# Kernel tuning notes

Measured on AMD Instinct MI355X. Metric: run time of the kernel, lower is better.

The kernel has to match this reference:

```python
import jax, jax.numpy as jnp
import numpy as np

N_NODES = 50000


def setup_inputs() -> dict:
    key = jax.random.key(0)
    k1, k2, k3, k4 = jax.random.split(key, 4)
    in_f, out_f = 128, 128
    n_edges = 625000
    x = jax.random.normal(k1, (N_NODES, in_f), dtype=jnp.float32)
    index = jax.random.randint(k2, (2, n_edges), 0, N_NODES, dtype=jnp.int64)
    # reset_parameters uses uniform(-1/sqrt(in), 1/sqrt(in))
    bound = 1.0 / np.sqrt(in_f)
    weight = jax.random.uniform(k3, (in_f, out_f), minval=-bound, maxval=bound, dtype=jnp.float32)
    bias = jax.random.uniform(k4, (out_f,), minval=-bound, maxval=bound, dtype=jnp.float32)
    return {"x": x, "index": index, "weight": weight, "bias": bias}


def reference(x, index, weight, bias):
    # F_out = D_hat^{-1/2} (A + I) D_hat^{-1/2} X W + b
    n = x.shape[0]
    loops = jnp.arange(n, dtype=index.dtype)
    src = jnp.concatenate([index[0], loops])  # [E + N]
    dst = jnp.concatenate([index[1], loops])
    # degrees of A_hat (counted on destination nodes)
    deg = jax.ops.segment_sum(jnp.ones_like(dst, dtype=x.dtype), dst, num_segments=n)
    dinv = jax.lax.rsqrt(jnp.maximum(deg, 1e-12))
    norm = dinv[src] * dinv[dst]  # [E + N]
    h = x @ weight  # [N, out] dense GEMM first (out <= in)
    msg = h[src] * norm[:, None]  # gather + scale
    out = jax.ops.segment_sum(msg, dst, num_segments=n)  # scatter-add
    return out + bias
```

## Files before the change

### kernel.cpp

```cpp
#include <hip/hip_runtime.h>

#define F   128
#define PAD 64

typedef short short8 __attribute__((ext_vector_type(8)));
typedef float f32x4v __attribute__((ext_vector_type(4)));

__device__ __forceinline__ ushort f2bf(float f) {
    uint b = __float_as_uint(f);
    uint r = (b + 0x7fffu + ((b >> 16) & 1u)) >> 16;
    return (ushort)r;
}
__device__ __forceinline__ float bflo(uint v) { return __uint_as_float(v << 16); }
__device__ __forceinline__ float bfhi(uint v) { return __uint_as_float(v & 0xffff0000u); }


__global__ __launch_bounds__(256) void prep(
    const float* __restrict__ w, ushort* __restrict__ wt,
    int* __restrict__ cnt, int n)
{
    int i = blockIdx.x * 256 + threadIdx.x;
    if (i < n) cnt[i] = 0;
    if (blockIdx.x == 0) {
        for (int idx = threadIdx.x; idx < F * 32; idx += 256) {
            int k = idx >> 5, c4 = idx & 31;
            float4 v = *reinterpret_cast<const float4*>(&w[k * F + c4 * 4]);
            wt[(c4 * 4 + 0) * F + k] = f2bf(v.x);
            wt[(c4 * 4 + 1) * F + k] = f2bf(v.y);
            wt[(c4 * 4 + 2) * F + k] = f2bf(v.z);
            wt[(c4 * 4 + 3) * F + k] = f2bf(v.w);
        }
    }
}


__global__ __launch_bounds__(256) void hybrid(
    const int* __restrict__ src, const int* __restrict__ dst, int ne,
    int* __restrict__ cnt, int* __restrict__ padded, int nbB,
    const float* __restrict__ x, const ushort* __restrict__ wt,
    ushort* __restrict__ g, int n)
{
    __shared__ ushort sX[64 * F];
    __shared__ ushort sW[F * F];

    if (blockIdx.x < nbB) {
        int base = (blockIdx.x * 256 + threadIdx.x) * 4;
        if (base + 3 < ne) {
            int4 s4 = *reinterpret_cast<const int4*>(&src[base]);
            int4 d4 = *reinterpret_cast<const int4*>(&dst[base]);
            int p;
            p = atomicAdd(&cnt[d4.x], 1); if (p < PAD) padded[(size_t)d4.x * PAD + p] = s4.x;
            p = atomicAdd(&cnt[d4.y], 1); if (p < PAD) padded[(size_t)d4.y * PAD + p] = s4.y;
            p = atomicAdd(&cnt[d4.z], 1); if (p < PAD) padded[(size_t)d4.z * PAD + p] = s4.z;
            p = atomicAdd(&cnt[d4.w], 1); if (p < PAD) padded[(size_t)d4.w * PAD + p] = s4.w;
        } else {
            for (int e = base; e < ne; ++e) {
                int s = src[e], d = dst[e];
                int p = atomicAdd(&cnt[d], 1);
                if (p < PAD) padded[(size_t)d * PAD + p] = s;
            }
        }
        return;
    }

    const int t    = threadIdx.x;
    const int lane = t & 63;
    const int wv   = t >> 6;
    const int row0 = (blockIdx.x - nbB) * 64;

    for (int i = t; i < 2048; i += 256) {
        int col = i >> 4, k8 = i & 15;
        short8 v = *reinterpret_cast<const short8*>(&wt[col * F + k8 * 8]);
        int byte = col * 256 + k8 * 16;
        byte ^= (col & 7) << 4;
        *reinterpret_cast<short8*>((char*)sW + byte) = v;
    }
    for (int i = t; i < 2048; i += 256) {
        int r = i >> 5, c4 = i & 31;
        int row = row0 + r;
        float4 v = make_float4(0.f, 0.f, 0.f, 0.f);
        if (row < n) v = *reinterpret_cast<const float4*>(&x[(size_t)row * F + c4 * 4]);
        ushort u[4] = {f2bf(v.x), f2bf(v.y), f2bf(v.z), f2bf(v.w)};
        int byte = r * 256 + c4 * 8;
        byte ^= (r & 7) << 4;
        *reinterpret_cast<uint2*>((char*)sX + byte) = *reinterpret_cast<uint2*>(u);
    }
    __syncthreads();

    const int l15 = lane & 15, kg = lane >> 4;

    short8 af[4][4];
    #pragma unroll
    for (int rt = 0; rt < 4; ++rt)
        #pragma unroll
        for (int kt = 0; kt < 4; ++kt) {
            int row = rt * 16 + l15;
            int byte = row * 256 + kt * 64 + kg * 16;
            byte ^= (row & 7) << 4;
            af[rt][kt] = *reinterpret_cast<const short8*>((const char*)sX + byte);
        }

    const int wc = wv * 32;
    short8 bfr[2][4];
    #pragma unroll
    for (int ct = 0; ct < 2; ++ct)
        #pragma unroll
        for (int kt = 0; kt < 4; ++kt) {
            int col = wc + ct * 16 + l15;
            int byte = col * 256 + kt * 64 + kg * 16;
            byte ^= (col & 7) << 4;
            bfr[ct][kt] = *reinterpret_cast<const short8*>((const char*)sW + byte);
        }

    f32x4v acc[4][2];
    #pragma unroll
    for (int rt = 0; rt < 4; ++rt)
        #pragma unroll
        for (int ct = 0; ct < 2; ++ct)
            acc[rt][ct] = (f32x4v){0.f, 0.f, 0.f, 0.f};

    #pragma unroll
    for (int kt = 0; kt < 4; ++kt)
        #pragma unroll
        for (int rt = 0; rt < 4; ++rt)
            #pragma unroll
            for (int ct = 0; ct < 2; ++ct)
                acc[rt][ct] = __builtin_amdgcn_mfma_f32_16x16x32_bf16(
                    af[rt][kt], bfr[ct][kt], acc[rt][ct], 0, 0, 0);

    #pragma unroll
    for (int rt = 0; rt < 4; ++rt) {
        int rbase = row0 + rt * 16 + kg * 4;
        #pragma unroll
        for (int ct = 0; ct < 2; ++ct) {
            int col = wc + ct * 16 + l15;
            #pragma unroll
            for (int rr = 0; rr < 4; ++rr) {
                int row = rbase + rr;
                if (row < n)
                    g[(size_t)row * F + col] = f2bf(acc[rt][ct][rr]);
            }
        }
    }
}


__global__ __launch_bounds__(256) void gather_bf16(
    const int* __restrict__ cnt, const int* __restrict__ padded,
    const ushort* __restrict__ g, const float* __restrict__ bias,
    float* __restrict__ out, int n)
{
    int wid  = (blockIdx.x * 256 + threadIdx.x) >> 6;
    int lane = threadIdx.x & 63;
    if (wid >= n) return;
    const int c = lane * 2;

    int   cv = cnt[wid];
    float dv = rsqrtf((float)cv + 1.0f);
    uint self = *reinterpret_cast<const uint*>(&g[(size_t)wid * F + c]);
    float ax = dv * bflo(self), ay = dv * bfhi(self);

    int m = cv < PAD ? cv : PAD;
    const int* pl = padded + (size_t)wid * PAD;

    int j = 0;
    for (; j + 4 <= m; j += 4) {
        int s0 = pl[j + 0], s1 = pl[j + 1], s2 = pl[j + 2], s3 = pl[j + 3];
        float d0 = rsqrtf((float)cnt[s0] + 1.0f);
        float d1 = rsqrtf((float)cnt[s1] + 1.0f);
        float d2 = rsqrtf((float)cnt[s2] + 1.0f);
        float d3 = rsqrtf((float)cnt[s3] + 1.0f);
        uint v0 = *reinterpret_cast<const uint*>(&g[(size_t)s0 * F + c]);
        uint v1 = *reinterpret_cast<const uint*>(&g[(size_t)s1 * F + c]);
        uint v2 = *reinterpret_cast<const uint*>(&g[(size_t)s2 * F + c]);
        uint v3 = *reinterpret_cast<const uint*>(&g[(size_t)s3 * F + c]);
        ax = fmaf(d0, bflo(v0), ax); ay = fmaf(d0, bfhi(v0), ay);
        ax = fmaf(d1, bflo(v1), ax); ay = fmaf(d1, bfhi(v1), ay);
        ax = fmaf(d2, bflo(v2), ax); ay = fmaf(d2, bfhi(v2), ay);
        ax = fmaf(d3, bflo(v3), ax); ay = fmaf(d3, bfhi(v3), ay);
    }
    for (; j < m; ++j) {
        int s = pl[j];
        float ds = rsqrtf((float)cnt[s] + 1.0f);
        uint v = *reinterpret_cast<const uint*>(&g[(size_t)s * F + c]);
        ax = fmaf(ds, bflo(v), ax);
        ay = fmaf(ds, bfhi(v), ay);
    }

    float2 bb = *reinterpret_cast<const float2*>(&bias[c]);
    float2 o;
    o.x = fmaf(dv, ax, bb.x);
    o.y = fmaf(dv, ay, bb.y);
    *reinterpret_cast<float2*>(&out[(size_t)wid * F + c]) = o;
}


__global__ __launch_bounds__(256) void gemm_scale(
    const float* __restrict__ x, const float* __restrict__ w,
    const float* __restrict__ dinv, float* __restrict__ g, int n)
{
    __shared__ float sWl[F * F];
    __shared__ float sXl[8][F];
    for (int i = threadIdx.x; i < F * F; i += 256) sWl[i] = w[i];
    __syncthreads();
    const int r  = threadIdx.x >> 5;
    const int cg = threadIdx.x & 31;
    for (int row0 = blockIdx.x * 8; row0 < n; row0 += gridDim.x * 8) {
        {
            int t4 = threadIdx.x * 4;
            int rr = t4 >> 7, cc = t4 & (F - 1);
            if (row0 + rr < n) {
                float4 v = *reinterpret_cast<const float4*>(&x[(size_t)(row0 + rr) * F + cc]);
                *reinterpret_cast<float4*>(&sXl[rr][cc]) = v;
            }
        }
        __syncthreads();
        int row = row0 + r;
        if (row < n) {
            float4 acc = make_float4(0.f, 0.f, 0.f, 0.f);
            const float* xr = sXl[r];
            #pragma unroll 8
            for (int k = 0; k < F; ++k) {
                float  xv = xr[k];
                float4 wv = *reinterpret_cast<const float4*>(&sWl[k * F + cg * 4]);
                acc.x = fmaf(xv, wv.x, acc.x);
                acc.y = fmaf(xv, wv.y, acc.y);
                acc.z = fmaf(xv, wv.z, acc.z);
                acc.w = fmaf(xv, wv.w, acc.w);
            }
            float s = dinv[row];
            acc.x *= s; acc.y *= s; acc.z *= s; acc.w *= s;
            *reinterpret_cast<float4*>(&g[(size_t)row * F + cg * 4]) = acc;
        }
        __syncthreads();
    }
}

__global__ void init_degf(float* __restrict__ deg, int n) {
    int i = blockIdx.x * blockDim.x + threadIdx.x;
    if (i < n) deg[i] = 1.0f;
}
__global__ void count_degf(const int* __restrict__ dst, int ne, float* __restrict__ deg) {
    int e = blockIdx.x * blockDim.x + threadIdx.x;
    if (e < ne) atomicAdd(&deg[dst[e]], 1.0f);
}
__global__ void calc_dinvf(const float* __restrict__ deg, float* __restrict__ dinv, int n) {
    int i = blockIdx.x * blockDim.x + threadIdx.x;
    if (i < n) dinv[i] = rsqrtf(fmaxf(deg[i], 1e-12f));
}
__global__ __launch_bounds__(256) void scatter_edges(
    const int* __restrict__ src, const int* __restrict__ dst, int ne,
    const float* __restrict__ g, float* __restrict__ out)
{
    int gid  = (blockIdx.x * blockDim.x + threadIdx.x) >> 5;
    int lane = threadIdx.x & 31;
    if (gid >= ne) return;
    int s = src[gid], d = dst[gid];
    float4 v = *reinterpret_cast<const float4*>(&g[(size_t)s * F + lane * 4]);
    float* op = &out[(size_t)d * F + lane * 4];
    atomicAdd(op + 0, v.x);
    atomicAdd(op + 1, v.y);
    atomicAdd(op + 2, v.z);
    atomicAdd(op + 3, v.w);
}
__global__ __launch_bounds__(256) void finalize(
    float* __restrict__ out, const float* __restrict__ g,
    const float* __restrict__ dinv, const float* __restrict__ bias, int n)
{
    int i = blockIdx.x * blockDim.x + threadIdx.x;
    if (i >= n * 32) return;
    int row = i >> 5, c4 = i & 31;
    float  s = dinv[row];
    float4 o = *reinterpret_cast<float4*>(&out[(size_t)i * 4]);
    float4 gg = *reinterpret_cast<const float4*>(&g[(size_t)i * 4]);
    float4 b = *reinterpret_cast<const float4*>(&bias[c4 * 4]);
    o.x = fmaf(s, o.x + gg.x, b.x);
    o.y = fmaf(s, o.y + gg.y, b.y);
    o.z = fmaf(s, o.z + gg.z, b.z);
    o.w = fmaf(s, o.w + gg.w, b.w);
    *reinterpret_cast<float4*>(&out[(size_t)i * 4]) = o;
}


extern "C" void kernel_launch(void* const* d_in, const int* in_sizes, int n_in,
                              void* d_out, int out_size, void* d_ws, size_t ws_size,
                              hipStream_t stream) {
    const float* x     = (const float*)d_in[0];
    const int*   index = (const int*)d_in[1];
    const float* w     = (const float*)d_in[2];
    const float* bias  = (const float*)d_in[3];
    float*       out   = (float*)d_out;

    int n  = in_sizes[0] / F;
    int ne = in_sizes[1] / 2;
    const int* src = index;
    const int* dst = index + ne;

    size_t e_cnt    = 0;
    size_t e_wt     = (e_cnt + n + 3) & ~(size_t)3;
    size_t e_padded = (e_wt + (F * F / 2) + 3) & ~(size_t)3;
    size_t e_g      = (e_padded + (size_t)n * PAD + 3) & ~(size_t)3;
    size_t need = (e_g + (size_t)n * (F / 2)) * 4;

    char* wsb = (char*)d_ws;
    int*    cnt    = (int*)wsb + e_cnt;
    ushort* wt     = (ushort*)((int*)wsb + e_wt);
    int*    padded = (int*)wsb + e_padded;
    ushort* g      = (ushort*)((int*)wsb + e_g);

    int nb  = (n + 255) / 256;
    int nbB = (ne / 4 + 255) / 256;
    int nbG = (n + 63) / 64;

    if (ws_size >= need) {
        prep<<<nb, 256, 0, stream>>>(w, wt, cnt, n);
        hybrid<<<nbB + nbG, 256, 0, stream>>>(src, dst, ne, cnt, padded, nbB, x, wt, g, n);
        int gb = (int)(((long long)n * 64 + 255) / 256);
        gather_bf16<<<gb, 256, 0, stream>>>(cnt, padded, g, bias, out, n);
    } else {
        float* degf  = (float*)wsb;
        float* dinvf = (float*)wsb + n;
        float* gf    = (float*)wsb + 2 * n;
        int nbE = (ne + 255) / 256;
        hipMemsetAsync(d_out, 0, (size_t)out_size * sizeof(float), stream);
        init_degf<<<nb, 256, 0, stream>>>(degf, n);
        count_degf<<<nbE, 256, 0, stream>>>(dst, ne, degf);
        calc_dinvf<<<nb, 256, 0, stream>>>(degf, dinvf, n);
        gemm_scale<<<(n + 7) / 8, 256, 0, stream>>>(x, w, dinvf, gf, n);
        int sc_blocks = (int)(((long long)ne * 32 + 255) / 256);
        scatter_edges<<<sc_blocks, 256, 0, stream>>>(src, dst, ne, gf, out);
        finalize<<<(n * 32 + 255) / 256, 256, 0, stream>>>(out, gf, dinvf, bias, n);
    }
}
```

Baseline: 101.4 us.

## Partition edge binning by XCD, store 16-bit neighbor ids, drop LDS in GEMM

The edge-binning blocks now each read a chunk of edges and only process destinations within one eighth of the node range, chosen by blockIdx mod 8. This keeps a node's atomics and padded-list writes on one XCD's L2. Neighbor ids in the padded adjacency are stored as ushort, which halves that traffic and is guarded by n <= 65535. The GEMM part loads x and wt straight from global memory into MFMA fragments with no LDS staging or barrier. The cost is that every edge is read eight times, and the GEMM loses operand reuse through shared memory.

```diff
diff --git a/kernel.cpp b/kernel.cpp
--- a/kernel.cpp
+++ b/kernel.cpp
@@ -1,7 +1,8 @@
 #include <hip/hip_runtime.h>
 
-#define F   128
-#define PAD 64
+#define F     128
+#define PAD   64
+#define CHUNK 8192
 
 typedef short short8 __attribute__((ext_vector_type(8)));
 typedef float f32x4v __attribute__((ext_vector_type(4)));
@@ -36,104 +37,101 @@
 
 __global__ __launch_bounds__(256) void hybrid(
     const int* __restrict__ src, const int* __restrict__ dst, int ne,
-    int* __restrict__ cnt, int* __restrict__ padded, int nbB,
+    int* __restrict__ cnt, ushort* __restrict__ padded, int nbB,
     const float* __restrict__ x, const ushort* __restrict__ wt,
     ushort* __restrict__ g, int n)
 {
-    __shared__ ushort sX[64 * F];
-    __shared__ ushort sW[F * F];
-
     if (blockIdx.x < nbB) {
-        int base = (blockIdx.x * 256 + threadIdx.x) * 4;
-        if (base + 3 < ne) {
-            int4 s4 = *reinterpret_cast<const int4*>(&src[base]);
-            int4 d4 = *reinterpret_cast<const int4*>(&dst[base]);
-            int p;
-            p = atomicAdd(&cnt[d4.x], 1); if (p < PAD) padded[(size_t)d4.x * PAD + p] = s4.x;
-            p = atomicAdd(&cnt[d4.y], 1); if (p < PAD) padded[(size_t)d4.y * PAD + p] = s4.y;
-            p = atomicAdd(&cnt[d4.z], 1); if (p < PAD) padded[(size_t)d4.z * PAD + p] = s4.z;
-            p = atomicAdd(&cnt[d4.w], 1); if (p < PAD) padded[(size_t)d4.w * PAD + p] = s4.w;
-        } else {
-            for (int e = base; e < ne; ++e) {
-                int s = src[e], d = dst[e];
-                int p = atomicAdd(&cnt[d], 1);
-                if (p < PAD) padded[(size_t)d * PAD + p] = s;
+        const int grp = blockIdx.x >> 3;
+        const int xcd = blockIdx.x & 7;
+        const int sh  = (n + 7) >> 3;
+        const int dlo = xcd * sh;
+        const int dhi = (dlo + sh) < n ? (dlo + sh) : n;
+        const int base = grp * CHUNK;
+        const int lim  = (base + CHUNK) < ne ? (base + CHUNK) : ne;
+        for (int e0 = base + threadIdx.x * 4; e0 < lim; e0 += 1024) {
+            if (e0 + 3 < lim) {
+                int4 s4 = *reinterpret_cast<const int4*>(&src[e0]);
+                int4 d4 = *reinterpret_cast<const int4*>(&dst[e0]);
+                if (d4.x >= dlo && d4.x < dhi) {
+                    int p = atomicAdd(&cnt[d4.x], 1);
+                    if (p < PAD) padded[(size_t)d4.x * PAD + p] = (ushort)s4.x;
+                }
+                if (d4.y >= dlo && d4.y < dhi) {
+                    int p = atomicAdd(&cnt[d4.y], 1);
+                    if (p < PAD) padded[(size_t)d4.y * PAD + p] = (ushort)s4.y;
+                }
+                if (d4.z >= dlo && d4.z < dhi) {
+                    int p = atomicAdd(&cnt[d4.z], 1);
+                    if (p < PAD) padded[(size_t)d4.z * PAD + p] = (ushort)s4.z;
+                }
+                if (d4.w >= dlo && d4.w < dhi) {
+                    int p = atomicAdd(&cnt[d4.w], 1);
+                    if (p < PAD) padded[(size_t)d4.w * PAD + p] = (ushort)s4.w;
+                }
+            } else {
+                for (int e = e0; e < lim; ++e) {
+                    int d = dst[e];
+                    if (d >= dlo && d < dhi) {
+                        int p = atomicAdd(&cnt[d], 1);
+                        if (p < PAD) padded[(size_t)d * PAD + p] = (ushort)src[e];
+                    }
+                }
             }
         }
         return;
     }
 
+    const int gb   = blockIdx.x - nbB;
     const int t    = threadIdx.x;
     const int lane = t & 63;
     const int wv   = t >> 6;
-    const int row0 = (blockIdx.x - nbB) * 64;
-
-    for (int i = t; i < 2048; i += 256) {
-        int col = i >> 4, k8 = i & 15;
-        short8 v = *reinterpret_cast<const short8*>(&wt[col * F + k8 * 8]);
-        int byte = col * 256 + k8 * 16;
-        byte ^= (col & 7) << 4;
-        *reinterpret_cast<short8*>((char*)sW + byte) = v;
-    }
-    for (int i = t; i < 2048; i += 256) {
-        int r = i >> 5, c4 = i & 31;
-        int row = row0 + r;
-        float4 v = make_float4(0.f, 0.f, 0.f, 0.f);
-        if (row < n) v = *reinterpret_cast<const float4*>(&x[(size_t)row * F + c4 * 4]);
-        ushort u[4] = {f2bf(v.x), f2bf(v.y), f2bf(v.z), f2bf(v.w)};
-        int byte = r * 256 + c4 * 8;
-        byte ^= (r & 7) << 4;
-        *reinterpret_cast<uint2*>((char*)sX + byte) = *reinterpret_cast<uint2*>(u);
-    }
-    __syncthreads();
-
-    const int l15 = lane & 15, kg = lane >> 4;
-
-    short8 af[4][4];
+    const int wr   = wv >> 1, wc = wv & 1;
+    const int l15  = lane & 15, kg = lane >> 4;
+    const int row0 = gb * 64 + wr * 32;
+    const int col0 = wc * 64;
+
+    f32x4v acc[2][4];
     #pragma unroll
-    for (int rt = 0; rt < 4; ++rt)
-        #pragma unroll
-        for (int kt = 0; kt < 4; ++kt) {
-            int row = rt * 16 + l15;
-            int byte = row * 256 + kt * 64 + kg * 16;
-            byte ^= (row & 7) << 4;
-            af[rt][kt] = *reinterpret_cast<const short8*>((const char*)sX + byte);
-        }
-
-    const int wc = wv * 32;
-    short8 bfr[2][4];
+    for (int rt = 0; rt < 2; ++rt)
+        #pragma unroll
+        for (int ct = 0; ct < 4; ++ct)
+            acc[rt][ct] = (f32x4v){0.f, 0.f, 0.f, 0.f};
+
     #pragma unroll
-    for (int ct = 0; ct < 2; ++ct)
-        #pragma unroll
-        for (int kt = 0; kt < 4; ++kt) {
-            int col = wc + ct * 16 + l15;
-            int byte = col * 256 + kt * 64 + kg * 16;
-            byte ^= (col & 7) << 4;
-            bfr[ct][kt] = *reinterpret_cast<const short8*>((const char*)sW + byte);
-        }
-
-    f32x4v acc[4][2];
+    for (int kt = 0; kt < 4; ++kt) {
+        const int k0 = kt * 32 + kg * 8;
+        short8 a[2];
+        #pragma unroll
+        for (int rt = 0; rt < 2; ++rt) {
+            int row = row0 + rt * 16 + l15;
+            row = row < n ? row : n - 1;
+            float4 p0 = *reinterpret_cast<const float4*>(&x[(size_t)row * F + k0]);
+            float4 p1 = *reinterpret_cast<const float4*>(&x[(size_t)row * F + k0 + 4]);
+            ushort u[8] = {f2bf(p0.x), f2bf(p0.y), f2bf(p0.z), f2bf(p0.w),
+                           f2bf(p1.x), f2bf(p1.y), f2bf(p1.z), f2bf(p1.w)};
+            a[rt] = *reinterpret_cast<short8*>(u);
+        }
+        short8 b[4];
+        #pragma unroll
+        for (int ct = 0; ct < 4; ++ct) {
+            int col = col0 + ct * 16 + l15;
+            b[ct] = *reinterpret_cast<const short8*>(&wt[col * F + k0]);
+        }
+        #pragma unroll
+        for (int rt = 0; rt < 2; ++rt)
+            #pragma unroll
+            for (int ct = 0; ct < 4; ++ct)
+                acc[rt][ct] = __builtin_amdgcn_mfma_f32_16x16x32_bf16(
+                    a[rt], b[ct], acc[rt][ct], 0, 0, 0);
+    }
+
     #pragma unroll
-    for (int rt = 0; rt < 4; ++rt)
-        #pragma unroll
-        for (int ct = 0; ct < 2; ++ct)
-            acc[rt][ct] = (f32x4v){0.f, 0.f, 0.f, 0.f};
-
-    #pragma unroll
-    for (int kt = 0; kt < 4; ++kt)
-        #pragma unroll
-        for (int rt = 0; rt < 4; ++rt)
-            #pragma unroll
-            for (int ct = 0; ct < 2; ++ct)
-                acc[rt][ct] = __builtin_amdgcn_mfma_f32_16x16x32_bf16(
-                    af[rt][kt], bfr[ct][kt], acc[rt][ct], 0, 0, 0);
-
-    #pragma unroll
-    for (int rt = 0; rt < 4; ++rt) {
+    for (int rt = 0; rt < 2; ++rt) {
         int rbase = row0 + rt * 16 + kg * 4;
         #pragma unroll
-        for (int ct = 0; ct < 2; ++ct) {
-            int col = wc + ct * 16 + l15;
+        for (int ct = 0; ct < 4; ++ct) {
+            int col = col0 + ct * 16 + l15;
             #pragma unroll
             for (int rr = 0; rr < 4; ++rr) {
                 int row = rbase + rr;
@@ -146,13 +144,14 @@
 
 
 __global__ __launch_bounds__(256) void gather_bf16(
-    const int* __restrict__ cnt, const int* __restrict__ padded,
+    const int* __restrict__ cnt, const ushort* __restrict__ padded,
     const ushort* __restrict__ g, const float* __restrict__ bias,
     float* __restrict__ out, int n)
 {
     int wid  = (blockIdx.x * 256 + threadIdx.x) >> 6;
     int lane = threadIdx.x & 63;
     if (wid >= n) return;
+    wid = __builtin_amdgcn_readfirstlane(wid);
     const int c = lane * 2;
 
     int   cv = cnt[wid];
@@ -161,7 +160,7 @@
     float ax = dv * bflo(self), ay = dv * bfhi(self);
 
     int m = cv < PAD ? cv : PAD;
-    const int* pl = padded + (size_t)wid * PAD;
+    const ushort* pl = padded + (size_t)wid * PAD;
 
     int j = 0;
     for (; j + 4 <= m; j += 4) {
@@ -296,23 +295,23 @@
     const int* src = index;
     const int* dst = index + ne;
 
-    size_t e_cnt    = 0;
-    size_t e_wt     = (e_cnt + n + 3) & ~(size_t)3;
-    size_t e_padded = (e_wt + (F * F / 2) + 3) & ~(size_t)3;
-    size_t e_g      = (e_padded + (size_t)n * PAD + 3) & ~(size_t)3;
-    size_t need = (e_g + (size_t)n * (F / 2)) * 4;
+    size_t b_cnt    = 0;
+    size_t b_wt     = (b_cnt + (size_t)n * 4 + 15) & ~(size_t)15;
+    size_t b_padded = (b_wt + (size_t)F * F * 2 + 15) & ~(size_t)15;
+    size_t b_g      = (b_padded + (size_t)n * PAD * 2 + 15) & ~(size_t)15;
+    size_t need     = b_g + (size_t)n * F * 2;
 
     char* wsb = (char*)d_ws;
-    int*    cnt    = (int*)wsb + e_cnt;
-    ushort* wt     = (ushort*)((int*)wsb + e_wt);
-    int*    padded = (int*)wsb + e_padded;
-    ushort* g      = (ushort*)((int*)wsb + e_g);
+    int*    cnt    = (int*)(wsb + b_cnt);
+    ushort* wt     = (ushort*)(wsb + b_wt);
+    ushort* padded = (ushort*)(wsb + b_padded);
+    ushort* g      = (ushort*)(wsb + b_g);
 
     int nb  = (n + 255) / 256;
-    int nbB = (ne / 4 + 255) / 256;
+    int nbB = ((ne + CHUNK - 1) / CHUNK) * 8;
     int nbG = (n + 63) / 64;
 
-    if (ws_size >= need) {
+    if (ws_size >= need && n <= 65535) {
         prep<<<nb, 256, 0, stream>>>(w, wt, cnt, n);
         hybrid<<<nbB + nbG, 256, 0, stream>>>(src, dst, ne, cnt, padded, nbB, x, wt, g, n);
         int gb = (int)(((long long)n * 64 + 255) / 256);
```

New measurement: 90.80 us. -10.5%, faster.
